# Optimization experiments

Measured on AMD Instinct MI355X. Metric: run time of the kernel, lower is better.

The kernel has to match this reference:

```python
import jax, jax.numpy as jnp
import numpy as np

V_MAX = 3.0
FEATURE_CLAMP = 10.0
TOP_K = 1


def _green_diag(d):
    """Diagonal of G = (tridiag(sub=1, diag=d, super=1))^{-1} for each batch row.
    d: (B, N) complex64. Stable two-sided continued-fraction (Thomas-like) recurrences:
      L_i = d_i - 1/L_{i-1},  U_i = d_i - 1/U_{i+1},  G_ii = 1/(L_i + U_i - d_i).
    Sequential over N (vectorized over B) via lax.scan.
    """
    dT = d.T  # (N, B)

    def step(c, di):
        nc = di - 1.0 / c
        return nc, nc

    L0 = dT[0]
    _, Lr = jax.lax.scan(step, L0, dT[1:])
    L = jnp.concatenate([L0[None], Lr], axis=0)  # (N, B)

    dR = dT[::-1]
    U0 = dR[0]
    _, Ur = jax.lax.scan(step, U0, dR[1:])
    U = jnp.concatenate([U0[None], Ur], axis=0)[::-1]  # (N, B)

    return (1.0 / (L + U - dT)).T  # (B, N)


def setup_inputs() -> dict:
    key = jax.random.key(0)
    B, N, D, E, F = 4, 4096, 512, 4, 2048
    ks = jax.random.split(key, 8)
    s = lambda k, sh, sc: (jax.random.normal(k, sh, jnp.float32) * sc)
    return dict(
        x=jax.random.normal(ks[0], (B, N, D), jnp.float32),
        v_proj_w=s(ks[1], (1, D), D ** -0.5),
        v_proj_b=jnp.zeros((1,), jnp.float32),
        gamma=jnp.float32(0.0),
        epsilon_param=jnp.float32(1.0),
        gate_w=s(ks[2], (E, D), D ** -0.5),
        gate_b=jnp.zeros((E,), jnp.float32),
        w1=s(ks[3], (E, D, F), D ** -0.5),
        b1=jnp.zeros((E, F), jnp.float32),
        w2=s(ks[4], (E, F, D), F ** -0.5),
        b2=jnp.zeros((E, D), jnp.float32),
        out_w=s(ks[5], (D, 2), 0.5),
        out_b=jnp.zeros((D,), jnp.float32),
        bk_scale=jnp.ones((D,), jnp.float32),
    )


def reference(x, v_proj_w, v_proj_b, gamma, epsilon_param, gate_w, gate_b,
              w1, b1, w2, b2, out_w, out_b, bk_scale):
    # 1) scalar potential from tokens
    v = jnp.einsum('bnd,od->bno', x, v_proj_w)[..., 0] + v_proj_b[0]  # (B, N)
    v = jnp.clip(v, -V_MAX, V_MAX)

    # 2) gamma-shifted complex tridiagonal Green's function diagonal
    eps = jax.nn.softplus(epsilon_param) + 1e-6
    z = 1j * (eps + gamma)                       # complex64 scalar
    d = ((v - 2.0).astype(jnp.complex64) - z)    # he_diag - z, (B, N)
    G = _green_diag(d)                            # (B, N) complex
    feats = jnp.clip(jnp.stack([G.real, G.imag], axis=-1), -FEATURE_CLAMP, FEATURE_CLAMP)  # (B,N,2)

    # 3) sparse MoE FFN (top-1 routing, experts = Linear -> GELU -> Linear)
    logits = jnp.einsum('bnd,ed->bne', x, gate_w) + gate_b
    probs = jax.nn.softmax(logits, axis=-1)
    top_p, top_i = jax.lax.top_k(probs, TOP_K)
    top_w = top_p / jnp.sum(top_p, axis=-1, keepdims=True)
    wmask = jnp.sum(jax.nn.one_hot(top_i, probs.shape[-1], dtype=probs.dtype) * top_w[..., None], axis=-2)  # (B,N,E)

    h = jax.nn.gelu(jnp.einsum('bnd,edf->benf', x, w1) + b1[None, :, None, :], approximate=False)
    y = jnp.einsum('benf,efd->bend', h, w2) + b2[None, :, None, :]
    ffn_out = jnp.einsum('bne,bend->bnd', wmask, y)

    # 4) combine spectral features with FFN output
    spec_out = jnp.einsum('bnc,dc->bnd', feats, out_w) + out_b
    return ffn_out + bk_scale * spec_out
```

## Files before the change

kernel.cpp:

```cpp
#include <hip/hip_runtime.h>
#include <hip/hip_bf16.h>
#include <math.h>


typedef __bf16 bf16x8 __attribute__((ext_vector_type(8)));
typedef float  f32x4  __attribute__((ext_vector_type(4)));
typedef __attribute__((address_space(3))) __bf16 lbf16;

#define B_   4
#define N_   4096
#define D_   512
#define E_   4
#define F_   2048
#define T_   (B_*N_)
#define CAP_ T_
#define R256 68
#define PADROWS (R256*256)

#define LGKM_BARRIER() asm volatile("s_waitcnt lgkmcnt(0)\n\ts_barrier" ::: "memory")

__device__ __forceinline__ void gload_lds16(const __bf16* g, lbf16* l) {
    __builtin_amdgcn_global_load_lds(
        (__attribute__((address_space(1))) void*)(void*)g,
        (__attribute__((address_space(3))) void*)l, 16, 0, 0);
}

__device__ __forceinline__ float fast_gelu(float x) {
    float u = 1.5957691216f * fmaf(0.044715f * x, x * x, x);
    return x / (1.0f + __expf(-u));
}

__device__ __forceinline__ void load8f2(const float2* p, float2* dst) {
    const float4* q = (const float4*)p;
    #pragma unroll
    for (int i = 0; i < 4; ++i) {
        float4 t = q[i];
        dst[2*i]   = make_float2(t.x, t.y);
        dst[2*i+1] = make_float2(t.z, t.w);
    }
}

__device__ __forceinline__ void mfma_tile(const char* Ab, const char* Bb,
                                          int cs0, int cs1, f32x4 acc[4][4]) {
    #pragma unroll
    for (int ks = 0; ks < 2; ++ks) {
        int cs = ks ? cs1 : cs0;
        bf16x8 af[4], bfr[4];
        #pragma unroll
        for (int m = 0; m < 4; ++m)
            af[m] = *(const bf16x8*)(Ab + m * 2048 + cs);
        #pragma unroll
        for (int n = 0; n < 4; ++n)
            bfr[n] = *(const bf16x8*)(Bb + n * 2048 + cs);
        #pragma unroll
        for (int m = 0; m < 4; ++m)
            #pragma unroll
            for (int n = 0; n < 4; ++n)
                acc[m][n] = __builtin_amdgcn_mfma_f32_16x16x32_bf16(af[m], bfr[n], acc[m][n], 0, 0, 0);
    }
}

__device__ alignas(256) __bf16 s_w1t[(size_t)E_*F_*D_];
__device__ alignas(256) __bf16 s_w2t[(size_t)E_*D_*F_];
__device__ alignas(256) __bf16 s_xl[(size_t)T_*D_];
__device__ alignas(256) __bf16 s_H[(size_t)PADROWS*F_];
__device__ alignas(256) float2 s_d[T_];
__device__ alignas(256) float2 s_feats[T_];
__device__ alignas(256) float2 s_L[T_];
__device__ alignas(256) float2 s_U[T_];
__device__ alignas(256) int    s_perm[E_*CAP_];
__device__ alignas(256) int    s_cnt[E_];
__device__ alignas(256) int    s_tpre[8];
__device__ alignas(256) int    s_eid[T_];

__device__ inline float dot8(float4 a, float4 b, float4 c, float4 d) {
    float s =      a.x * c.x;
    s = fmaf(a.y, c.y, s); s = fmaf(a.z, c.z, s); s = fmaf(a.w, c.w, s);
    s = fmaf(b.x, d.x, s); s = fmaf(b.y, d.y, s); s = fmaf(b.z, d.z, s);
    s = fmaf(b.w, d.w, s);
    return s;
}

__device__ inline float wave_sum(float s) {
    #pragma unroll
    for (int off = 32; off > 0; off >>= 1) s += __shfl_xor(s, off);
    return s;
}

__global__ __launch_bounds__(256) void prep_trans_kernel(
        const float* __restrict__ w1, const float* __restrict__ w2,
        __bf16* __restrict__ w1t, __bf16* __restrict__ w2t,
        const float* __restrict__ x,
        const float* __restrict__ vw, const float* __restrict__ vb,
        const float* __restrict__ gamma, const float* __restrict__ epsp,
        const float* __restrict__ gw, const float* __restrict__ gb,
        float2* __restrict__ dbuf, int* __restrict__ eid,
        __bf16* __restrict__ xlin) {
    __shared__ alignas(16) float tile[32][33];
    int idx = blockIdx.x;
    int tid = threadIdx.x;
    if (idx < 8192) {
        int which = idx >> 12;
        int r = idx & 4095;
        int e = r >> 10;
        int t = r & 1023;
        int R, C, c0, r0;
        const float* s;
        __bf16* d;
        if (which == 0) { R = D_; C = F_; c0 = (t & 63) * 32; r0 = (t >> 6) * 32;
                          s = w1 + (size_t)e * R * C; d = w1t + (size_t)e * R * C; }
        else            { R = F_; C = D_; c0 = (t & 15) * 32; r0 = (t >> 4) * 32;
                          s = w2 + (size_t)e * R * C; d = w2t + (size_t)e * R * C; }
        int tx = tid & 31, ty = tid >> 5;
        #pragma unroll
        for (int i = 0; i < 4; ++i)
            tile[ty + i*8][tx] = s[(size_t)(r0 + ty + i*8) * C + c0 + tx];
        __syncthreads();
        #pragma unroll
        for (int i = 0; i < 4; ++i)
            d[(size_t)(c0 + ty + i*8) * R + r0 + tx] = (__bf16)tile[tx][ty + i*8];
    } else {
        int wv = tid >> 6, lane = tid & 63;
        int token = (idx - 8192) * 4 + wv;
        const float4* xr = (const float4*)(x + (size_t)token * D_);
        float4 xa = xr[lane*2], xb = xr[lane*2 + 1];

        bf16x8 xv = {(__bf16)xa.x,(__bf16)xa.y,(__bf16)xa.z,(__bf16)xa.w,
                     (__bf16)xb.x,(__bf16)xb.y,(__bf16)xb.z,(__bf16)xb.w};
        *(bf16x8*)(xlin + (size_t)token * D_ + lane * 8) = xv;

        const float4* vr = (const float4*)vw;
        float sv = dot8(xa, xb, vr[lane*2], vr[lane*2 + 1]);
        float sg0, sg1, sg2, sg3;
        {
            const float4* g0 = (const float4*)(gw + 0*D_);
            const float4* g1 = (const float4*)(gw + 1*D_);
            const float4* g2 = (const float4*)(gw + 2*D_);
            const float4* g3 = (const float4*)(gw + 3*D_);
            sg0 = dot8(xa, xb, g0[lane*2], g0[lane*2+1]);
            sg1 = dot8(xa, xb, g1[lane*2], g1[lane*2+1]);
            sg2 = dot8(xa, xb, g2[lane*2], g2[lane*2+1]);
            sg3 = dot8(xa, xb, g3[lane*2], g3[lane*2+1]);
        }
        sv  = wave_sum(sv);
        sg0 = wave_sum(sg0); sg1 = wave_sum(sg1);
        sg2 = wave_sum(sg2); sg3 = wave_sum(sg3);

        if (lane == 0) {
            float v = sv + vb[0];
            v = fminf(fmaxf(v, -3.0f), 3.0f);
            float eps = log1pf(expf(epsp[0])) + 1e-6f;
            dbuf[token] = make_float2(v - 2.0f, -(eps + gamma[0]));

            float l0 = sg0 + gb[0], l1 = sg1 + gb[1], l2 = sg2 + gb[2], l3 = sg3 + gb[3];
            float best = l0; int be = 0;
            if (l1 > best) { best = l1; be = 1; }
            if (l2 > best) { best = l2; be = 2; }
            if (l3 > best) { best = l3; be = 3; }
            eid[token] = be;
        }
    }
}

__global__ __launch_bounds__(1024) void route_scan_kernel(
        const int* __restrict__ eid, int* __restrict__ perm,
        int* __restrict__ cnt, int* __restrict__ tpre,
        const float2* __restrict__ dbuf, float2* __restrict__ Lb,
        float2* __restrict__ Ub, float2* __restrict__ feats) {
    int tid = threadIdx.x;
    if (blockIdx.x == 0) {
        __shared__ int chunkcnt[256][4];
        __shared__ int chunkoff[256][4];
        __shared__ int totals[4];
        int wv = tid >> 6, lane = tid & 63;

        for (int c = wv; c < 256; c += 16) {
            int e = eid[c * 64 + lane];
            unsigned long long m0 = __ballot(e == 0);
            unsigned long long m1 = __ballot(e == 1);
            unsigned long long m2 = __ballot(e == 2);
            unsigned long long m3 = __ballot(e == 3);
            if (lane == 0) {
                chunkcnt[c][0] = __popcll(m0);
                chunkcnt[c][1] = __popcll(m1);
                chunkcnt[c][2] = __popcll(m2);
                chunkcnt[c][3] = __popcll(m3);
            }
        }
        __syncthreads();

        if (wv < 4) {
            int e = wv, carry = 0;
            #pragma unroll
            for (int g = 0; g < 4; ++g) {
                int idx = g * 64 + lane;
                int v = chunkcnt[idx][e];
                int s = v;
                #pragma unroll
                for (int off = 1; off < 64; off <<= 1) {
                    int u = __shfl_up(s, off);
                    if (lane >= off) s += u;
                }
                chunkoff[idx][e] = carry + s - v;
                carry += __shfl(s, 63);
            }
            if (lane == 0) { cnt[e] = carry; totals[e] = carry; }
        }
        __syncthreads();
        if (tid == 0) {
            int acc = 0;
            #pragma unroll
            for (int e = 0; e < E_; ++e) { tpre[e] = acc; acc += (totals[e] + 255) >> 8; }
            tpre[4] = acc;
        }

        for (int c = wv; c < 256; c += 16) {
            int t = c * 64 + lane;
            int e = eid[t];
            unsigned long long m0 = __ballot(e == 0);
            unsigned long long m1 = __ballot(e == 1);
            unsigned long long m2 = __ballot(e == 2);
            unsigned long long m3 = __ballot(e == 3);
            unsigned long long mym = (e == 0) ? m0 : (e == 1) ? m1 : (e == 2) ? m2 : m3;
            unsigned long long below = lane ? (mym & ((1ull << lane) - 1ull)) : 0ull;
            int pos = chunkoff[c][e] + __popcll(below);
            perm[e * CAP_ + pos] = t;
        }
    } else {
        __shared__ alignas(16) float chunkM[8][64][8];
        __shared__ alignas(16) float bound[8][64][4];
        int s = tid >> 6, c = tid & 63;
        int b = s & 3, dir = (s >> 2) & 1;

        if (tid < 512) {
            float ar=1, ai=0, br=0, bi=0, cr=0, ci=0, dr=1, di=0;
            float2 cur[8], nxt[8];
            {
                int seq0 = c * 64;
                const float2* p = dbuf + (dir ? (b*N_ + N_ - 8 - seq0) : (b*N_ + seq0));
                load8f2(p, cur);
            }
            for (int g = 0; g < 8; ++g) {
                if (g < 7) {
                    int seq0 = c * 64 + (g + 1) * 8;
                    const float2* p = dbuf + (dir ? (b*N_ + N_ - 8 - seq0) : (b*N_ + seq0));
                    load8f2(p, nxt);
                }
                #pragma unroll
                for (int q = 0; q < 8; ++q) {
                    float2 dv = dir ? cur[7 - q] : cur[q];
                    float nar = dv.x*ar - dv.y*ai - cr;
                    float nai = dv.x*ai + dv.y*ar - ci;
                    float nbr = dv.x*br - dv.y*bi - dr;
                    float nbi = dv.x*bi + dv.y*br - di;
                    cr = ar; ci = ai; dr = br; di = bi;
                    ar = nar; ai = nai; br = nbr; bi = nbi;
                }
                float m = fmaxf(fmaxf(fmaxf(fabsf(ar),fabsf(ai)),fmaxf(fabsf(br),fabsf(bi))),
                                fmaxf(fmaxf(fabsf(cr),fabsf(ci)),fmaxf(fabsf(dr),fabsf(di))));
                float inv = 1.0f / fmaxf(m, 1e-30f);
                ar*=inv; ai*=inv; br*=inv; bi*=inv; cr*=inv; ci*=inv; dr*=inv; di*=inv;
                #pragma unroll
                for (int q = 0; q < 8; ++q) cur[q] = nxt[q];
            }
            float* cm = chunkM[s][c];
            cm[0]=ar; cm[1]=ai; cm[2]=br; cm[3]=bi; cm[4]=cr; cm[5]=ci; cm[6]=dr; cm[7]=di;
        }
        __syncthreads();

        if (tid < 8) {
            int ss = tid;
            float pr=1, pi=0, qr=0, qi=0;
            for (int cc = 0; cc < 64; ++cc) {
                float* bd = bound[ss][cc];
                bd[0]=pr; bd[1]=pi; bd[2]=qr; bd[3]=qi;
                const float* m = chunkM[ss][cc];
                float npr = m[0]*pr - m[1]*pi + m[2]*qr - m[3]*qi;
                float npi = m[0]*pi + m[1]*pr + m[2]*qi + m[3]*qr;
                float nqr = m[4]*pr - m[5]*pi + m[6]*qr - m[7]*qi;
                float nqi = m[4]*pi + m[5]*pr + m[6]*qi + m[7]*qr;
                float mx = fmaxf(fmaxf(fabsf(npr),fabsf(npi)), fmaxf(fabsf(nqr),fabsf(nqi)));
                float inv = 1.0f / fmaxf(mx, 1e-30f);
                pr = npr*inv; pi = npi*inv; qr = nqr*inv; qi = nqi*inv;
            }
        }
        __syncthreads();

        if (tid < 512) {
            const float* bd = bound[s][c];
            float pr=bd[0], pi=bd[1], qr=bd[2], qi=bd[3];
            float den = fmaxf(pr*pr + pi*pi, 1e-30f);
            float invr = (qr*pr + qi*pi) / den;
            float invi = (qi*pr - qr*pi) / den;
            float2 cur[8], nxt[8];
            {
                int seq0 = c * 64;
                const float2* p = dbuf + (dir ? (b*N_ + N_ - 8 - seq0) : (b*N_ + seq0));
                load8f2(p, cur);
            }
            for (int g = 0; g < 8; ++g) {
                if (g < 7) {
                    int seq0 = c * 64 + (g + 1) * 8;
                    const float2* p = dbuf + (dir ? (b*N_ + N_ - 8 - seq0) : (b*N_ + seq0));
                    load8f2(p, nxt);
                }
                #pragma unroll
                for (int q = 0; q < 8; ++q) {
                    int seq = c * 64 + g * 8 + q;
                    int orig = dir ? (N_ - 1 - seq) : seq;
                    int t = b * N_ + orig;
                    float2 dv = dir ? cur[7 - q] : cur[q];
                    float Lr = dv.x - invr, Li = dv.y - invi;
                    if (dir) Ub[t] = make_float2(Lr, Li);
                    else     Lb[t] = make_float2(Lr, Li);
                    float d2 = Lr*Lr + Li*Li;
                    invr = Lr / d2; invi = -Li / d2;
                }
                #pragma unroll
                for (int q = 0; q < 8; ++q) cur[q] = nxt[q];
            }
        }
        __threadfence();
        __syncthreads();

        for (int t = tid; t < T_; t += 1024) {
            float2 L = Lb[t], U = Ub[t], dv = dbuf[t];
            float sr = L.x + U.x - dv.x;
            float si = L.y + U.y - dv.y;
            float den = sr*sr + si*si;
            float Gr = sr / den, Gi = -si / den;
            Gr = fminf(fmaxf(Gr, -10.0f), 10.0f);
            Gi = fminf(fmaxf(Gi, -10.0f), 10.0f);
            feats[t] = make_float2(Gr, Gi);
        }
    }
}

__global__ __launch_bounds__(512, 4) void gemm1_kernel(
        const __bf16* __restrict__ xlin, const __bf16* __restrict__ w1t,
        const float* __restrict__ b1, __bf16* __restrict__ Hb,
        const int* __restrict__ tpre, const int* __restrict__ cnt_p,
        const int* __restrict__ perm) {
    int bid = blockIdx.x;
    int lb  = (bid & 7) * 136 + (bid >> 3);
    int rt = lb >> 4, ct = lb & 15;
    if (rt >= tpre[4]) return;
    int e = 0;
    #pragma unroll
    for (int k = 1; k < E_; ++k) if (rt >= tpre[k]) e = k;
    int cnt = cnt_p[e];
    int base = tpre[e] * 256;

    __shared__ __bf16 A[256 * 64];
    __shared__ __bf16 Bm[128 * 64];

    int tid = threadIdx.x, lane = tid & 63, wv = tid >> 6;
    int fl = lane & 15, gl = lane >> 4;
    int wr = wv >> 1, wc = wv & 1;

    int r8    = lane >> 3;
    int scolb = ((lane & 7) * 16) ^ (r8 << 4);
    const __bf16* aS[4];
    #pragma unroll
    for (int i = 0; i < 4; ++i) {
        int gr = rt * 256 + wv * 32 + r8 + i * 8;
        int il = gr - base;
        int token = (il < cnt) ? perm[e * CAP_ + il] : 0;
        aS[i] = xlin + (size_t)token * D_ + (scolb >> 1);
    }
    const __bf16* bS0 = w1t + (size_t)(e * F_ + ct * 128 + wv * 16 + r8) * 512 + (scolb >> 1);
    lbf16* aD0 = (lbf16*)A  + wv * 32 * 64;
    lbf16* bD0 = (lbf16*)Bm + wv * 16 * 64;

    int xorv = (fl & 7) << 4;
    int cs0 = (gl * 16) ^ xorv;
    int cs1 = (64 + gl * 16) ^ xorv;
    const char* Ab = (const char*)A  + (wr * 64 + fl) * 128;
    const char* Bb = (const char*)Bm + (wc * 64 + fl) * 128;

    f32x4 acc[4][4];
    #pragma unroll
    for (int m = 0; m < 4; ++m)
        #pragma unroll
        for (int n = 0; n < 4; ++n) acc[m][n] = (f32x4){0.f,0.f,0.f,0.f};

    #pragma unroll
    for (int i = 0; i < 4; ++i)
        gload_lds16(aS[i], aD0 + i * 512);
    #pragma unroll
    for (int i = 0; i < 2; ++i)
        gload_lds16(bS0 + (size_t)i * 8 * 512, bD0 + i * 512);

    for (int kt = 0; kt < 8; ++kt) {
        __syncthreads();
        mfma_tile(Ab, Bb, cs0, cs1, acc);
        if (kt + 1 < 8) {
            LGKM_BARRIER();
            #pragma unroll
            for (int i = 0; i < 4; ++i)
                gload_lds16(aS[i] + (kt + 1) * 64, aD0 + i * 512);
            #pragma unroll
            for (int i = 0; i < 2; ++i)
                gload_lds16(bS0 + (size_t)i * 8 * 512 + (kt + 1) * 64, bD0 + i * 512);
        }
    }

    int gre = rt * 256 + wr * 64;
    int gce = ct * 128 + wc * 64;
    float b1v[4];
    #pragma unroll
    for (int n = 0; n < 4; ++n) b1v[n] = b1[e * F_ + gce + n*16 + fl];
    #pragma unroll
    for (int m = 0; m < 4; ++m)
        #pragma unroll
        for (int r = 0; r < 4; ++r) {
            __bf16* hrow = Hb + (size_t)(gre + m*16 + gl*4 + r) * F_ + gce;
            #pragma unroll
            for (int n = 0; n < 4; ++n)
                hrow[n*16 + fl] = (__bf16)fast_gelu(acc[m][n][r] + b1v[n]);
        }
}

__global__ __launch_bounds__(512, 4) void gemm2_kernel(
        const __bf16* __restrict__ Hb, const __bf16* __restrict__ w2t,
        const float* __restrict__ b2, const float* __restrict__ outw,
        const float* __restrict__ outb, const float* __restrict__ bk,
        const float2* __restrict__ feats, const int* __restrict__ perm,
        const int* __restrict__ cnt_p, const int* __restrict__ tpre,
        float* __restrict__ out) {
    int bid = blockIdx.x;
    int lb  = (bid & 7) * 34 + (bid >> 3);
    int rt = lb >> 2, ct = lb & 3;
    if (rt >= tpre[4]) return;
    int e = 0;
    #pragma unroll
    for (int k = 1; k < E_; ++k) if (rt >= tpre[k]) e = k;

    __shared__ __bf16 A[256 * 64];
    __shared__ __bf16 Bm[128 * 64];

    int tid = threadIdx.x, lane = tid & 63, wv = tid >> 6;
    int fl = lane & 15, gl = lane >> 4;
    int wr = wv >> 1, wc = wv & 1;

    int r8    = lane >> 3;
    int scolb = ((lane & 7) * 16) ^ (r8 << 4);
    const __bf16* aS0 = Hb  + (size_t)(rt * 256 + wv * 32 + r8) * F_ + (scolb >> 1);
    const __bf16* bS0 = w2t + (size_t)(e * D_ + ct * 128 + wv * 16 + r8) * F_ + (scolb >> 1);
    lbf16* aD0 = (lbf16*)A  + wv * 32 * 64;
    lbf16* bD0 = (lbf16*)Bm + wv * 16 * 64;

    int xorv = (fl & 7) << 4;
    int cs0 = (gl * 16) ^ xorv;
    int cs1 = (64 + gl * 16) ^ xorv;
    const char* Ab = (const char*)A  + (wr * 64 + fl) * 128;
    const char* Bb = (const char*)Bm + (wc * 64 + fl) * 128;

    f32x4 acc[4][4];
    #pragma unroll
    for (int m = 0; m < 4; ++m)
        #pragma unroll
        for (int n = 0; n < 4; ++n) acc[m][n] = (f32x4){0.f,0.f,0.f,0.f};

    #pragma unroll
    for (int i = 0; i < 4; ++i)
        gload_lds16(aS0 + (size_t)i * 8 * F_, aD0 + i * 512);
    #pragma unroll
    for (int i = 0; i < 2; ++i)
        gload_lds16(bS0 + (size_t)i * 8 * F_, bD0 + i * 512);

    for (int kt = 0; kt < 32; ++kt) {
        __syncthreads();
        mfma_tile(Ab, Bb, cs0, cs1, acc);
        if (kt + 1 < 32) {
            LGKM_BARRIER();
            #pragma unroll
            for (int i = 0; i < 4; ++i)
                gload_lds16(aS0 + (size_t)i * 8 * F_ + (kt + 1) * 64, aD0 + i * 512);
            #pragma unroll
            for (int i = 0; i < 2; ++i)
                gload_lds16(bS0 + (size_t)i * 8 * F_ + (kt + 1) * 64, bD0 + i * 512);
        }
    }

    int cnt = cnt_p[e];
    int ibase = rt * 256 + wr * 64 - tpre[e] * 256;
    int gce = ct * 128 + wc * 64;
    float c_b2[4], c_o0[4], c_o1[4], c_ob[4], c_bk[4];
    #pragma unroll
    for (int n = 0; n < 4; ++n) {
        int dcol = gce + n*16 + fl;
        c_b2[n] = b2[e * D_ + dcol];
        c_o0[n] = outw[dcol * 2 + 0];
        c_o1[n] = outw[dcol * 2 + 1];
        c_ob[n] = outb[dcol];
        c_bk[n] = bk[dcol];
    }
    #pragma unroll
    for (int m = 0; m < 4; ++m)
        #pragma unroll
        for (int r = 0; r < 4; ++r) {
            int i = ibase + m*16 + gl*4 + r;
            if (i >= cnt) continue;
            int token = perm[e * CAP_ + i];
            float2 ft = feats[token];
            float* orow = out + (size_t)token * D_;
            #pragma unroll
            for (int n = 0; n < 4; ++n) {
                int dcol = gce + n*16 + fl;
                float spec = ft.x * c_o0[n] + ft.y * c_o1[n] + c_ob[n];
                orow[dcol] = acc[m][n][r] + c_b2[n] + c_bk[n] * spec;
            }
        }
}

extern "C" void kernel_launch(void* const* d_in, const int* in_sizes, int n_in,
                              void* d_out, int out_size, void* d_ws, size_t ws_size,
                              hipStream_t stream) {
    const float* x     = (const float*)d_in[0];
    const float* vpw   = (const float*)d_in[1];
    const float* vpb   = (const float*)d_in[2];
    const float* gamma = (const float*)d_in[3];
    const float* epsp  = (const float*)d_in[4];
    const float* gw    = (const float*)d_in[5];
    const float* gb    = (const float*)d_in[6];
    const float* w1    = (const float*)d_in[7];
    const float* b1    = (const float*)d_in[8];
    const float* w2    = (const float*)d_in[9];
    const float* b2    = (const float*)d_in[10];
    const float* ow    = (const float*)d_in[11];
    const float* ob    = (const float*)d_in[12];
    const float* bk    = (const float*)d_in[13];
    float* out = (float*)d_out;

    const size_t szW  = (size_t)E_ * F_ * D_ * sizeof(__bf16);
    const size_t szF2 = (size_t)T_ * sizeof(float2);
    const size_t szPm = (size_t)E_ * CAP_ * sizeof(int);
    const size_t szCt = 256;
    const size_t szXl = (size_t)T_ * D_ * sizeof(__bf16);
    const size_t szH  = (size_t)PADROWS * F_ * sizeof(__bf16);
    const size_t szEi = (size_t)T_ * sizeof(int);
    size_t need = 2*szW + 4*szF2 + szPm + 2*szCt + szXl + szH + szEi + 16*256;

    __bf16 *w1t, *w2t, *xlin, *Hbuf; float2 *dbuf, *Lb, *Ub, *feats;
    int *perm, *cnt, *tpre, *eid;
    int use_ws = (d_ws != nullptr && ws_size >= need);
    if (use_ws) {
        size_t off = 0;
        auto carve = [&](size_t bytes) {
            void* p = (char*)d_ws + off;
            off += (bytes + 255) & ~(size_t)255;
            return p;
        };
        w1t   = (__bf16*)carve(szW);
        w2t   = (__bf16*)carve(szW);
        xlin  = (__bf16*)carve(szXl);
        Hbuf  = (__bf16*)carve(szH);
        dbuf  = (float2*)carve(szF2);
        Lb    = (float2*)carve(szF2);
        Ub    = (float2*)carve(szF2);
        feats = (float2*)carve(szF2);
        perm  = (int*)   carve(szPm);
        cnt   = (int*)   carve(szCt);
        tpre  = (int*)   carve(szCt);
        eid   = (int*)   carve(szEi);
    } else {
        void* p;
        hipGetSymbolAddress(&p, HIP_SYMBOL(s_w1t));  w1t   = (__bf16*)p;
        hipGetSymbolAddress(&p, HIP_SYMBOL(s_w2t));  w2t   = (__bf16*)p;
        hipGetSymbolAddress(&p, HIP_SYMBOL(s_xl));   xlin  = (__bf16*)p;
        hipGetSymbolAddress(&p, HIP_SYMBOL(s_H));    Hbuf  = (__bf16*)p;
        hipGetSymbolAddress(&p, HIP_SYMBOL(s_d));    dbuf  = (float2*)p;
        hipGetSymbolAddress(&p, HIP_SYMBOL(s_L));    Lb    = (float2*)p;
        hipGetSymbolAddress(&p, HIP_SYMBOL(s_U));    Ub    = (float2*)p;
        hipGetSymbolAddress(&p, HIP_SYMBOL(s_feats));feats = (float2*)p;
        hipGetSymbolAddress(&p, HIP_SYMBOL(s_perm)); perm  = (int*)p;
        hipGetSymbolAddress(&p, HIP_SYMBOL(s_cnt));  cnt   = (int*)p;
        hipGetSymbolAddress(&p, HIP_SYMBOL(s_tpre)); tpre  = (int*)p;
        hipGetSymbolAddress(&p, HIP_SYMBOL(s_eid));  eid   = (int*)p;
    }

    prep_trans_kernel<<<12288, 256, 0, stream>>>(w1, w2, w1t, w2t,
                                                 x, vpw, vpb, gamma, epsp, gw, gb,
                                                 dbuf, eid, xlin);
    route_scan_kernel<<<2, 1024, 0, stream>>>(eid, perm, cnt, tpre, dbuf, Lb, Ub, feats);
    gemm1_kernel<<<R256*16, 512, 0, stream>>>(xlin, w1t, b1, Hbuf, tpre, cnt, perm);
    gemm2_kernel<<<R256*4, 512, 0, stream>>>(Hbuf, w2t, b2, ow, ob, bk,
                                             feats, perm, cnt, tpre, out);
}
```

Before: 194.7 us.

## Double-buffer gemm1 LDS tiles with K=32 steps to overlap loads and MFMA

Reworks the gemm1 main loop from a single 64-wide K tile buffer into two 32-wide K buffers. The global-to-LDS load for the next K step is issued before the MFMAs on the current buffer. The goal is to hide global load latency behind compute instead of stalling on it each iteration. In exchange there are twice as many barriers and vmcnt waits, and the XOR swizzle is dropped, so LDS bank conflicts may rise.

```diff
diff --git a/kernel.cpp b/kernel.cpp
--- a/kernel.cpp
+++ b/kernel.cpp
@@ -18,6 +18,7 @@
 #define PADROWS (R256*256)
 
 #define LGKM_BARRIER() asm volatile("s_waitcnt lgkmcnt(0)\n\ts_barrier" ::: "memory")
+#define VM0_BARRIER()  asm volatile("s_waitcnt vmcnt(0)\n\ts_barrier" ::: "memory")
 
 __device__ __forceinline__ void gload_lds16(const __bf16* g, lbf16* l) {
     __builtin_amdgcn_global_load_lds(
@@ -58,6 +59,22 @@
             for (int n = 0; n < 4; ++n)
                 acc[m][n] = __builtin_amdgcn_mfma_f32_16x16x32_bf16(af[m], bfr[n], acc[m][n], 0, 0, 0);
     }
+}
+
+__device__ __forceinline__ void mfma_step32(const char* Ab, const char* Bb,
+                                            int gl16, f32x4 acc[4][4]) {
+    bf16x8 af[4], bfr[4];
+    #pragma unroll
+    for (int m = 0; m < 4; ++m)
+        af[m] = *(const bf16x8*)(Ab + m * 1024 + gl16);
+    #pragma unroll
+    for (int n = 0; n < 4; ++n)
+        bfr[n] = *(const bf16x8*)(Bb + n * 1024 + gl16);
+    #pragma unroll
+    for (int m = 0; m < 4; ++m)
+        #pragma unroll
+        for (int n = 0; n < 4; ++n)
+            acc[m][n] = __builtin_amdgcn_mfma_f32_16x16x32_bf16(af[m], bfr[n], acc[m][n], 0, 0, 0);
 }
 
 __device__ alignas(256) __bf16 s_w1t[(size_t)E_*F_*D_];
@@ -351,32 +368,32 @@
     int cnt = cnt_p[e];
     int base = tpre[e] * 256;
 
-    __shared__ __bf16 A[256 * 64];
-    __shared__ __bf16 Bm[128 * 64];
+    __shared__ __bf16 A[2][256 * 32];
+    __shared__ __bf16 Bm[2][128 * 32];
 
     int tid = threadIdx.x, lane = tid & 63, wv = tid >> 6;
     int fl = lane & 15, gl = lane >> 4;
     int wr = wv >> 1, wc = wv & 1;
 
-    int r8    = lane >> 3;
-    int scolb = ((lane & 7) * 16) ^ (r8 << 4);
-    const __bf16* aS[4];
-    #pragma unroll
-    for (int i = 0; i < 4; ++i) {
-        int gr = rt * 256 + wv * 32 + r8 + i * 8;
+    int srow = tid >> 2;
+    int selc = (tid & 3) * 8;
+    const __bf16* aS[2];
+    #pragma unroll
+    for (int i = 0; i < 2; ++i) {
+        int gr = rt * 256 + srow + i * 128;
         int il = gr - base;
         int token = (il < cnt) ? perm[e * CAP_ + il] : 0;
-        aS[i] = xlin + (size_t)token * D_ + (scolb >> 1);
-    }
-    const __bf16* bS0 = w1t + (size_t)(e * F_ + ct * 128 + wv * 16 + r8) * 512 + (scolb >> 1);
-    lbf16* aD0 = (lbf16*)A  + wv * 32 * 64;
-    lbf16* bD0 = (lbf16*)Bm + wv * 16 * 64;
-
-    int xorv = (fl & 7) << 4;
-    int cs0 = (gl * 16) ^ xorv;
-    int cs1 = (64 + gl * 16) ^ xorv;
-    const char* Ab = (const char*)A  + (wr * 64 + fl) * 128;
-    const char* Bb = (const char*)Bm + (wc * 64 + fl) * 128;
+        aS[i] = xlin + (size_t)token * D_ + selc;
+    }
+    const __bf16* bS0 = w1t + (size_t)(e * F_ + ct * 128 + srow) * 512 + selc;
+    lbf16* aD[2] = { (lbf16*)A[0] + wv * 512, (lbf16*)A[1] + wv * 512 };
+    lbf16* bD[2] = { (lbf16*)Bm[0] + wv * 512, (lbf16*)Bm[1] + wv * 512 };
+
+    int gl16 = gl * 16;
+    const char* Ab[2] = { (const char*)A[0]  + (wr * 64 + fl) * 64,
+                          (const char*)A[1]  + (wr * 64 + fl) * 64 };
+    const char* Bb[2] = { (const char*)Bm[0] + (wc * 64 + fl) * 64,
+                          (const char*)Bm[1] + (wc * 64 + fl) * 64 };
 
     f32x4 acc[4][4];
     #pragma unroll
@@ -384,25 +401,21 @@
         #pragma unroll
         for (int n = 0; n < 4; ++n) acc[m][n] = (f32x4){0.f,0.f,0.f,0.f};
 
-    #pragma unroll
-    for (int i = 0; i < 4; ++i)
-        gload_lds16(aS[i], aD0 + i * 512);
-    #pragma unroll
-    for (int i = 0; i < 2; ++i)
-        gload_lds16(bS0 + (size_t)i * 8 * 512, bD0 + i * 512);
-
-    for (int kt = 0; kt < 8; ++kt) {
-        __syncthreads();
-        mfma_tile(Ab, Bb, cs0, cs1, acc);
-        if (kt + 1 < 8) {
-            LGKM_BARRIER();
-            #pragma unroll
-            for (int i = 0; i < 4; ++i)
-                gload_lds16(aS[i] + (kt + 1) * 64, aD0 + i * 512);
-            #pragma unroll
-            for (int i = 0; i < 2; ++i)
-                gload_lds16(bS0 + (size_t)i * 8 * 512 + (kt + 1) * 64, bD0 + i * 512);
-        }
+    gload_lds16(aS[0], aD[0]);
+    gload_lds16(aS[1], aD[0] + 4096);
+    gload_lds16(bS0, bD[0]);
+
+    #pragma unroll
+    for (int kt = 0; kt < 16; ++kt) {
+        int cur = kt & 1, nxt = cur ^ 1;
+        VM0_BARRIER();
+        __builtin_amdgcn_sched_barrier(0);
+        if (kt + 1 < 16) {
+            gload_lds16(aS[0] + (kt + 1) * 32, aD[nxt]);
+            gload_lds16(aS[1] + (kt + 1) * 32, aD[nxt] + 4096);
+            gload_lds16(bS0 + (kt + 1) * 32, bD[nxt]);
+        }
+        mfma_step32(Ab[cur], Bb[cur], gl16, acc);
     }
 
     int gre = rt * 256 + wr * 64;
```

Measured after the change: 195.6 us. About the same (+0.5%).
